# Performance work log

Hardware: AMD Instinct MI355X
Metric: run time of the kernel (lower is better)

The kernel has to match this reference:

```python
import math
import jax, jax.numpy as jnp
import numpy as np

DIM_IN = 2048
DIM_OUT = 2048
BLOCK = 128
N_BLOCKS = 256
SPARSITY = 0.1
BATCH = 8192


def setup_inputs() -> dict:
    key = jax.random.key(0)
    k1, k2, k3, k4, k5 = jax.random.split(key, 5)
    x = jax.random.normal(k1, (BATCH, DIM_IN), dtype=jnp.float32)
    weight = jax.random.normal(k2, (DIM_IN, DIM_OUT), dtype=jnp.float32) * (1.0 / math.sqrt(DIM_IN))
    bias = jax.random.normal(k3, (DIM_OUT,), dtype=jnp.float32) * 0.01
    gate_w = jax.random.normal(k4, (DIM_IN, N_BLOCKS), dtype=jnp.float32) * (1.0 / math.sqrt(DIM_IN))
    gate_b = jax.random.normal(k5, (N_BLOCKS,), dtype=jnp.float32) * 0.01
    return {"x": x, "weight": weight, "bias": bias, "gate_w": gate_w, "gate_b": gate_b}


def _sparsify1d(g):
    # k-th largest kept per row; threshold, mask, renormalize (Sparsify1D)
    n = g.shape[-1]
    k = int(math.ceil(SPARSITY * n))
    topval = jax.lax.top_k(g, k)[0][:, -1:]          # (B, 1) k-th largest value
    res = jnp.where(g >= topval, g, jnp.zeros_like(g))
    return res / (jnp.sum(res, axis=-1, keepdims=True) / n)


def reference(x, weight, bias, gate_w, gate_b):
    B = x.shape[0]
    s = DIM_IN // BLOCK                               # 16 block-rows/cols
    # gate network: Linear -> Sparsify1D
    g = _sparsify1d(x @ gate_w + gate_b)              # (B, s*s)
    gb = g.reshape(B, s, s)                           # (B, s_in, s_out)
    xb = x.reshape(B, s, BLOCK)                       # (B, s_in, block)
    Wb = weight.reshape(s, BLOCK, s, BLOCK)           # (s_in, block, s_out, block)
    # gated block matrix-vector multiply:
    # y[b,q,n] = sum_{p,m} g[b,p,q] * x[b,p,m] * W[p,m,q,n]
    y = jnp.einsum('bpq,bpm,pmqn->bqn', gb, xb, Wb)
    return y.reshape(B, DIM_OUT) + bias
```

## Files before the change

### kernel.cpp

```cpp
#include <hip/hip_runtime.h>
#include <hip/hip_bf16.h>
#include <stdint.h>

#define BATCH  8192
#define DIN    2048
#define DOUT   2048
#define NB     256
#define KSEL   26
#define GDELTA 1e-4f

typedef __attribute__((ext_vector_type(4))) float f32x4;
typedef __attribute__((ext_vector_type(8))) __bf16 bf16x8;
typedef __attribute__((ext_vector_type(8))) unsigned short u16x8;

__device__ __forceinline__ float bf2f(unsigned short u){
  union { unsigned int i; float f; } v; v.i = ((unsigned int)u) << 16; return v.f;
}
__device__ __forceinline__ unsigned short f2bf_c(float f){
  __bf16 b = (__bf16)f;
  union { __bf16 b; unsigned short u; } v; v.b = b; return v.u;
}
__device__ __forceinline__ void gload16(const unsigned short* g, unsigned short* l){
  __builtin_amdgcn_global_load_lds(
      (const __attribute__((address_space(1))) void*)g,
      (__attribute__((address_space(3))) void*)l, 16, 0, 0);
}


__global__ __launch_bounds__(256) void conv_wt2(const float* __restrict__ w,
                                                unsigned short* __restrict__ wtt)
{
  __shared__ float tl[64][65];
  const int k0 = blockIdx.x * 64;
  const int n0 = blockIdx.y * 64;
  const int c  = threadIdx.x & 63;
  const int r4 = threadIdx.x >> 6;
  #pragma unroll
  for (int i = 0; i < 16; i++){
    const int r = r4 * 16 + i;
    tl[r][c] = w[(size_t)(k0 + r) * DOUT + n0 + c];
  }
  __syncthreads();
  const int n  = threadIdx.x & 63;
  const int cp = threadIdx.x >> 6;
  const int gn = n0 + n;
  const size_t base = ((size_t)(gn >> 7) * 32 + (k0 >> 6)) * 8192 + (size_t)(gn & 127) * 64;
  const int sw = gn & 7;
  #pragma unroll
  for (int u = 0; u < 2; u++){
    const int cc = cp * 2 + u;
    u16x8 o;
    #pragma unroll
    for (int j = 0; j < 8; j++) o[j] = f2bf_c(tl[cc * 8 + j][n]);
    *(u16x8*)&wtt[base + ((cc ^ sw) << 3)] = o;
  }
}

__global__ __launch_bounds__(256) void conv_gwt2(const float* __restrict__ gw,
    unsigned short* __restrict__ ght, unsigned short* __restrict__ glt)
{
  __shared__ float tl[64][65];
  const int k0 = blockIdx.x * 64;
  const int c0 = blockIdx.y * 64;
  const int c  = threadIdx.x & 63;
  const int r4 = threadIdx.x >> 6;
  #pragma unroll
  for (int i = 0; i < 16; i++){
    const int r = r4 * 16 + i;
    tl[r][c] = gw[(size_t)(k0 + r) * NB + c0 + c];
  }
  __syncthreads();
  const int n  = threadIdx.x & 63;
  const int cp = threadIdx.x >> 6;
  const size_t base = ((size_t)(c0 >> 6) * 32 + (k0 >> 6)) * 4096 + (size_t)n * 64;
  const int sw = n & 7;
  #pragma unroll
  for (int u = 0; u < 2; u++){
    const int cc = cp * 2 + u;
    u16x8 hi, lo;
    #pragma unroll
    for (int j = 0; j < 8; j++){
      const float v = tl[cc * 8 + j][n];
      const __bf16 hb = (__bf16)v;
      union { __bf16 b; unsigned short u; } uh; uh.b = hb;
      hi[j] = uh.u;
      lo[j] = f2bf_c(v - (float)hb);
    }
    const int off = (cc ^ sw) << 3;
    *(u16x8*)&ght[base + off] = hi;
    *(u16x8*)&glt[base + off] = lo;
  }
}

__global__ __launch_bounds__(256) void gate_v3(
    const float* __restrict__ x,
    const unsigned short* __restrict__ ght,
    const unsigned short* __restrict__ glt,
    float* __restrict__ part,
    unsigned short* __restrict__ xbt)
{
  __shared__ unsigned short Axh[128 * 64], Axl[128 * 64];
  __shared__ unsigned short Bh[2][64 * 64], Bl[2][64 * 64];

  const int b0   = blockIdx.x * 128;
  const int ct   = blockIdx.y;
  const int z    = blockIdx.z;
  const int ks0  = z * 16;
  const int t    = threadIdx.x;
  const int lane = t & 63;
  const int wid  = t >> 6;
  const int bw   = wid & 1;
  const int cw   = wid >> 1;
  const int l15  = lane & 15;
  const int l4   = lane >> 4;
  const bool emit = (blockIdx.y == 0);

  const int ar  = t >> 1;
  const int ah4 = (t & 1) * 4;

  f32x4 acc[4][2];
  #pragma unroll
  for (int m = 0; m < 4; m++)
    #pragma unroll
    for (int n = 0; n < 2; n++) acc[m][n] = (f32x4)0.0f;

  int aoff[2][4], boff[2][2];
  #pragma unroll
  for (int ksi = 0; ksi < 2; ksi++){
    const int chunk = ksi * 4 + l4;
    #pragma unroll
    for (int m = 0; m < 4; m++){
      const int row = bw * 64 + m * 16 + l15;
      aoff[ksi][m] = row * 64 + ((chunk ^ (row & 7)) << 3);
    }
    #pragma unroll
    for (int n = 0; n < 2; n++){
      const int row = cw * 32 + n * 16 + l15;
      boff[ksi][n] = row * 64 + ((chunk ^ (row & 7)) << 3);
    }
  }

  f32x4 xr[8];
  auto LOADX = [&](int s){
    const float* xp = &x[(size_t)(b0 + ar) * DIN + (size_t)(ks0 + s) * 64 + ah4 * 8];
    #pragma unroll
    for (int j = 0; j < 8; j++) xr[j] = ((const f32x4*)xp)[j];
  };
  auto GLOADB = [&](int bb, int s){
    const size_t base = ((size_t)ct * 32 + (ks0 + s)) * 4096;
    #pragma unroll
    for (int i = 0; i < 2; i++){
      const int slot = (wid * 2 + i) * 512;
      gload16(ght + base + slot + lane * 8, &Bh[bb][slot]);
      gload16(glt + base + slot + lane * 8, &Bl[bb][slot]);
    }
  };
  auto WRITEA = [&](int s){
    const int sw = ar & 7;
    const size_t gb = ((size_t)(b0 >> 7) * 32 + (ks0 + s)) * 8192 + (size_t)ar * 64;
    #pragma unroll
    for (int j = 0; j < 4; j++){
      u16x8 hi, lo;
      #pragma unroll
      for (int e = 0; e < 8; e++){
        const float v = xr[j * 2 + (e >> 2)][e & 3];
        const __bf16 hb = (__bf16)v;
        union { __bf16 b; unsigned short u; } uh; uh.b = hb;
        hi[e] = uh.u;
        lo[e] = f2bf_c(v - (float)hb);
      }
      const int c8 = ((ah4 + j) ^ sw) << 3;
      *(u16x8*)&Axh[ar * 64 + c8] = hi;
      *(u16x8*)&Axl[ar * 64 + c8] = lo;
      if (emit) *(u16x8*)&xbt[gb + c8] = hi;
    }
  };

  GLOADB(0, 0);
  LOADX(0);
  int buf = 0;
  #pragma unroll 1
  for (int s = 0; s < 16; s++){
    __syncthreads();
    WRITEA(s);
    __syncthreads();
    if (s < 15){ GLOADB(buf ^ 1, s + 1); LOADX(s + 1); }
    #pragma unroll
    for (int ksi = 0; ksi < 2; ksi++){
      bf16x8 ah[4], al[4], bh[2], bl[2];
      #pragma unroll
      for (int m = 0; m < 4; m++){
        ah[m] = *(const bf16x8*)&Axh[aoff[ksi][m]];
        al[m] = *(const bf16x8*)&Axl[aoff[ksi][m]];
      }
      #pragma unroll
      for (int n = 0; n < 2; n++){
        bh[n] = *(const bf16x8*)&Bh[buf][boff[ksi][n]];
        bl[n] = *(const bf16x8*)&Bl[buf][boff[ksi][n]];
      }
      #pragma unroll
      for (int m = 0; m < 4; m++)
        #pragma unroll
        for (int n = 0; n < 2; n++){
          acc[m][n] = __builtin_amdgcn_mfma_f32_16x16x32_bf16(ah[m], bh[n], acc[m][n], 0, 0, 0);
          acc[m][n] = __builtin_amdgcn_mfma_f32_16x16x32_bf16(al[m], bh[n], acc[m][n], 0, 0, 0);
          acc[m][n] = __builtin_amdgcn_mfma_f32_16x16x32_bf16(ah[m], bl[n], acc[m][n], 0, 0, 0);
        }
    }
    buf ^= 1;
  }

  float* dst = part + (size_t)z * BATCH * NB;
  #pragma unroll
  for (int m = 0; m < 4; m++){
    const int brow = b0 + bw * 64 + m * 16 + l4 * 4;
    #pragma unroll
    for (int n = 0; n < 2; n++){
      const int ccol = ct * 64 + cw * 32 + n * 16 + l15;
      #pragma unroll
      for (int r = 0; r < 4; r++)
        dst[(size_t)(brow + r) * NB + ccol] = acc[m][n][r];
    }
  }
}

__global__ __launch_bounds__(256) void topk(float* __restrict__ part,
    const float* __restrict__ gb, int* __restrict__ flags)
{
  const int lane = threadIdx.x & 63;
  const int row  = blockIdx.x * 4 + (threadIdx.x >> 6);
  f32x4* p0 = (f32x4*)&part[(size_t)row * NB];
  const f32x4* p1 = (const f32x4*)&part[(size_t)(BATCH + row) * NB];
  const f32x4* gbv = (const f32x4*)gb;
  f32x4 v = p0[lane] + p1[lane] + gbv[lane];

  const float NEG = -3.402823466e38f;
  float w0 = v[0], w1 = v[1], w2 = v[2], w3 = v[3];
  float thr = 0.f, nxt = 0.f;
  for (int it = 0; it < KSEL + 1; it++){
    float lm = fmaxf(fmaxf(w0, w1), fmaxf(w2, w3));
    float wm = lm;
    #pragma unroll
    for (int off = 32; off; off >>= 1) wm = fmaxf(wm, __shfl_xor(wm, off, 64));
    unsigned long long ball = __ballot(lm == wm);
    int first = __ffsll(ball) - 1;
    if (lane == first){
      if      (w0 == wm) w0 = NEG;
      else if (w1 == wm) w1 = NEG;
      else if (w2 == wm) w2 = NEG;
      else               w3 = NEG;
    }
    if (it < KSEL) thr = wm; else nxt = wm;
  }
  if (lane == 0) flags[row] = (thr - nxt < GDELTA) ? 1 : 0;

  float s = 0.f;
  #pragma unroll
  for (int j = 0; j < 4; j++) s += (v[j] >= thr) ? v[j] : 0.f;
  #pragma unroll
  for (int off = 32; off; off >>= 1) s += __shfl_xor(s, off, 64);
  const float d = s * (1.0f / NB);
  f32x4 o;
  #pragma unroll
  for (int j = 0; j < 4; j++) o[j] = (v[j] >= thr) ? v[j] / d : 0.f;
  p0[lane] = o;
}

__global__ __launch_bounds__(256) void refine(
    const float* __restrict__ x, const float* __restrict__ gw,
    const float* __restrict__ gb, const int* __restrict__ flags,
    float* __restrict__ part)
{
  const int lane = threadIdx.x & 63;
  const int row  = blockIdx.x * 4 + (threadIdx.x >> 6);
  if (!flags[row]) return;

  f32x4 acc0 = (f32x4)0.f, acc1 = (f32x4)0.f;
  const float* xp = &x[(size_t)row * DIN];
  #pragma unroll 8
  for (int k = 0; k < 1024; k++){
    const float xv = xp[k];
    const f32x4 wv = *(const f32x4*)&gw[(size_t)k * NB + lane * 4];
    #pragma unroll
    for (int j = 0; j < 4; j++) acc0[j] = fmaf(xv, wv[j], acc0[j]);
  }
  #pragma unroll 8
  for (int k = 1024; k < 2048; k++){
    const float xv = xp[k];
    const f32x4 wv = *(const f32x4*)&gw[(size_t)k * NB + lane * 4];
    #pragma unroll
    for (int j = 0; j < 4; j++) acc1[j] = fmaf(xv, wv[j], acc1[j]);
  }
  const f32x4 gbv = *(const f32x4*)&gb[lane * 4];
  f32x4 v;
  #pragma unroll
  for (int j = 0; j < 4; j++) v[j] = acc0[j] + acc1[j] + gbv[j];

  const float NEG = -3.402823466e38f;
  float w0 = v[0], w1 = v[1], w2 = v[2], w3 = v[3];
  float thr = 0.f;
  for (int it = 0; it < KSEL; it++){
    float lm = fmaxf(fmaxf(w0, w1), fmaxf(w2, w3));
    float wm = lm;
    #pragma unroll
    for (int off = 32; off; off >>= 1) wm = fmaxf(wm, __shfl_xor(wm, off, 64));
    unsigned long long ball = __ballot(lm == wm);
    int first = __ffsll(ball) - 1;
    if (lane == first){
      if      (w0 == wm) w0 = NEG;
      else if (w1 == wm) w1 = NEG;
      else if (w2 == wm) w2 = NEG;
      else               w3 = NEG;
    }
    thr = wm;
  }
  float s = 0.f;
  #pragma unroll
  for (int j = 0; j < 4; j++) s += (v[j] >= thr) ? v[j] : 0.f;
  #pragma unroll
  for (int off = 32; off; off >>= 1) s += __shfl_xor(s, off, 64);
  const float d = s * (1.0f / NB);
  f32x4 o;
  #pragma unroll
  for (int j = 0; j < 4; j++) o[j] = (v[j] >= thr) ? v[j] / d : 0.f;
  *(f32x4*)&part[(size_t)row * NB + lane * 4] = o;
}

__global__ __launch_bounds__(256) void main_v3(
    const unsigned short* __restrict__ xbt,
    const unsigned short* __restrict__ wtt,
    const float* __restrict__ g,
    const float* __restrict__ bias,
    float* __restrict__ out)
{
  __shared__ unsigned short XA[2][128 * 64], WB[2][128 * 64];
  __shared__ float gl[128 * 17];

  const int f  = blockIdx.x;
  const int q  = f >> 6;
  const int bt = (f & 7) * 8 + ((f >> 3) & 7);
  const int b0 = bt * 128;
  const int t    = threadIdx.x;
  const int lane = t & 63;
  const int wid  = t >> 6;
  const int wr   = (wid >> 1) * 64;
  const int wc   = (wid & 1) * 64;
  const int l15  = lane & 15;
  const int l4   = lane >> 4;

  for (int e = t; e < 128 * 16; e += 256){
    const int r = e >> 4, p = e & 15;
    gl[r * 17 + p] = g[(size_t)(b0 + r) * NB + p * 16 + q];
  }

  f32x4 accT[4][4], accP[4][4];
  #pragma unroll
  for (int m = 0; m < 4; m++)
    #pragma unroll
    for (int n = 0; n < 4; n++){ accT[m][n] = (f32x4)0.0f; accP[m][n] = (f32x4)0.0f; }

  int aoff[2][4], boff[2][4];
  #pragma unroll
  for (int ksi = 0; ksi < 2; ksi++){
    const int chunk = ksi * 4 + l4;
    #pragma unroll
    for (int m = 0; m < 4; m++){
      const int row = wr + m * 16 + l15;
      aoff[ksi][m] = row * 64 + ((chunk ^ (row & 7)) << 3);
    }
    #pragma unroll
    for (int n = 0; n < 4; n++){
      const int row = wc + n * 16 + l15;
      boff[ksi][n] = row * 64 + ((chunk ^ (row & 7)) << 3);
    }
  }

  const unsigned short* asrc0 = xbt + (size_t)bt * 32 * 8192;
  const unsigned short* bsrc0 = wtt + (size_t)q  * 32 * 8192;

  auto GLOAD = [&](int bb, int kp){
    const unsigned short* as = asrc0 + (size_t)kp * 8192;
    const unsigned short* bs = bsrc0 + (size_t)kp * 8192;
    #pragma unroll
    for (int i = 0; i < 4; i++){
      const int slot = (wid * 4 + i) * 512;
      gload16(as + slot + lane * 8, &XA[bb][slot]);
      gload16(bs + slot + lane * 8, &WB[bb][slot]);
    }
  };

  GLOAD(0, 0);
  int buf = 0;
  #pragma unroll 1
  for (int kp = 0; kp < 32; kp++){
    __syncthreads();
    if (kp < 31) GLOAD(buf ^ 1, kp + 1);
    #pragma unroll
    for (int ksi = 0; ksi < 2; ksi++){
      bf16x8 a[4], b[4];
      #pragma unroll
      for (int m = 0; m < 4; m++) a[m] = *(const bf16x8*)&XA[buf][aoff[ksi][m]];
      #pragma unroll
      for (int n = 0; n < 4; n++) b[n] = *(const bf16x8*)&WB[buf][boff[ksi][n]];
      #pragma unroll
      for (int m = 0; m < 4; m++)
        #pragma unroll
        for (int n = 0; n < 4; n++)
          accP[m][n] = __builtin_amdgcn_mfma_f32_16x16x32_bf16(a[m], b[n], accP[m][n], 0, 0, 0);
    }
    if (kp & 1){
      const int p = kp >> 1;
      #pragma unroll
      for (int m = 0; m < 4; m++){
        const int rb = wr + m * 16 + l4 * 4;
        f32x4 g4;
        #pragma unroll
        for (int r = 0; r < 4; r++) g4[r] = gl[(rb + r) * 17 + p];
        #pragma unroll
        for (int n = 0; n < 4; n++){
          accT[m][n] += g4 * accP[m][n];
          accP[m][n] = (f32x4)0.0f;
        }
      }
    }
    buf ^= 1;
  }

  #pragma unroll
  for (int n = 0; n < 4; n++){
    const int col = q * 128 + wc + n * 16 + l15;
    const float bv = bias[col];
    #pragma unroll
    for (int m = 0; m < 4; m++){
      #pragma unroll
      for (int r = 0; r < 4; r++){
        const int row = b0 + wr + m * 16 + l4 * 4 + r;
        out[(size_t)row * DOUT + col] = accT[m][n][r] + bv;
      }
    }
  }
}

extern "C" void kernel_launch(void* const* d_in, const int* in_sizes, int n_in,
                              void* d_out, int out_size, void* d_ws, size_t ws_size,
                              hipStream_t stream)
{
  const float* x    = (const float*)d_in[0];
  const float* w    = (const float*)d_in[1];
  const float* bias = (const float*)d_in[2];
  const float* gw   = (const float*)d_in[3];
  const float* gb   = (const float*)d_in[4];
  float* out = (float*)d_out;

  char* wsb = (char*)d_ws;
  float*          part = (float*)wsb;
  unsigned short* wtt  = (unsigned short*)(wsb + (size_t)8  * 1024 * 1024);
  unsigned short* xbt  = (unsigned short*)(wsb + (size_t)16 * 1024 * 1024);
  unsigned short* ght  = (unsigned short*)(wsb + (size_t)48 * 1024 * 1024);
  unsigned short* glt  = (unsigned short*)(wsb + (size_t)49 * 1024 * 1024);
  int*            flg  = (int*)           (wsb + (size_t)50 * 1024 * 1024);

  conv_gwt2<<<dim3(DIN / 64, NB / 64), 256, 0, stream>>>(gw, ght, glt);
  gate_v3  <<<dim3(BATCH / 128, 4, 2), 256, 0, stream>>>(x, ght, glt, part, xbt);
  topk     <<<BATCH / 4, 256, 0, stream>>>(part, gb, flg);
  refine   <<<BATCH / 4, 256, 0, stream>>>(x, gw, gb, flg, part);
  conv_wt2 <<<dim3(DIN / 64, DOUT / 64), 256, 0, stream>>>(w, wtt);
  main_v3  <<<1024, 256, 0, stream>>>(xbt, wtt, part, bias, out);
}
```

Baseline: 288.3 us.

## Pre-split x into bf16 hi/lo tiles and switch to 32-wide K tiles

Adds a separate conversion kernel that splits x into bf16 hi and lo tiles in a swizzled 32-wide K layout, storing the lo part temporarily in the output buffer. The gate GEMM then streams both operands with direct global-to-LDS loads instead of converting in registers, which removes one barrier per step. All tiled layouts (weight, gate weight, x) move to 32-element K chunks with a new swizzle. The main kernel applies the gate per 128-wide block through a transposed gate tile in LDS, read as one vector load. In exchange it adds a kernel launch, an extra global round trip for the x lo part, and twice as many K iterations with smaller tiles.

```diff
diff --git a/kernel.cpp b/kernel.cpp
--- a/kernel.cpp
+++ b/kernel.cpp
@@ -27,6 +27,37 @@
 }
 
 
+__global__ __launch_bounds__(256) void conv_xhl(const float* __restrict__ x,
+    unsigned short* __restrict__ xht, unsigned short* __restrict__ xlt)
+{
+  const int r    = threadIdx.x >> 2;
+  const int cq   = threadIdx.x & 3;
+  const int grow = blockIdx.x * 64 + r;
+  const int kp   = (blockIdx.y << 2) + cq;
+  const int lrow = grow & 127;
+  const int sw   = (lrow >> 1) & 3;
+  const size_t base = ((size_t)(grow >> 7) * 64 + kp) * 4096 + lrow * 32;
+  const float* xp = &x[(size_t)grow * DIN + kp * 32];
+  #pragma unroll
+  for (int c3 = 0; c3 < 4; c3++){
+    f32x4 a0 = *(const f32x4*)(xp + c3 * 8);
+    f32x4 a1 = *(const f32x4*)(xp + c3 * 8 + 4);
+    u16x8 hi, lo;
+    #pragma unroll
+    for (int j = 0; j < 4; j++){
+      const __bf16 h0 = (__bf16)a0[j];
+      const __bf16 h1 = (__bf16)a1[j];
+      union { __bf16 b; unsigned short u; } u0, u1; u0.b = h0; u1.b = h1;
+      hi[j] = u0.u; hi[4 + j] = u1.u;
+      lo[j]     = f2bf_c(a0[j] - (float)h0);
+      lo[4 + j] = f2bf_c(a1[j] - (float)h1);
+    }
+    const int off = (c3 ^ sw) << 3;
+    *(u16x8*)&xht[base + off] = hi;
+    *(u16x8*)&xlt[base + off] = lo;
+  }
+}
+
 __global__ __launch_bounds__(256) void conv_wt2(const float* __restrict__ w,
                                                 unsigned short* __restrict__ wtt)
 {
@@ -44,15 +75,18 @@
   const int n  = threadIdx.x & 63;
   const int cp = threadIdx.x >> 6;
   const int gn = n0 + n;
-  const size_t base = ((size_t)(gn >> 7) * 32 + (k0 >> 6)) * 8192 + (size_t)(gn & 127) * 64;
-  const int sw = gn & 7;
+  const int q  = gn >> 7;
+  const int ln = gn & 127;
+  const int sw = (ln >> 1) & 3;
   #pragma unroll
   for (int u = 0; u < 2; u++){
     const int cc = cp * 2 + u;
+    const int kp = (k0 >> 5) + (cc >> 2);
+    const int c3 = cc & 3;
     u16x8 o;
     #pragma unroll
     for (int j = 0; j < 8; j++) o[j] = f2bf_c(tl[cc * 8 + j][n]);
-    *(u16x8*)&wtt[base + ((cc ^ sw) << 3)] = o;
+    *(u16x8*)&wtt[((size_t)q * 64 + kp) * 4096 + ln * 32 + ((c3 ^ sw) << 3)] = o;
   }
 }
 
@@ -70,42 +104,45 @@
     tl[r][c] = gw[(size_t)(k0 + r) * NB + c0 + c];
   }
   __syncthreads();
-  const int n  = threadIdx.x & 63;
+  const int ln = threadIdx.x & 63;
   const int cp = threadIdx.x >> 6;
-  const size_t base = ((size_t)(c0 >> 6) * 32 + (k0 >> 6)) * 4096 + (size_t)n * 64;
-  const int sw = n & 7;
+  const int ct = blockIdx.y;
+  const int sw = (ln >> 1) & 3;
   #pragma unroll
   for (int u = 0; u < 2; u++){
     const int cc = cp * 2 + u;
+    const int kp = (k0 >> 5) + (cc >> 2);
+    const int c3 = cc & 3;
     u16x8 hi, lo;
     #pragma unroll
     for (int j = 0; j < 8; j++){
-      const float v = tl[cc * 8 + j][n];
+      const float v = tl[cc * 8 + j][ln];
       const __bf16 hb = (__bf16)v;
       union { __bf16 b; unsigned short u; } uh; uh.b = hb;
       hi[j] = uh.u;
       lo[j] = f2bf_c(v - (float)hb);
     }
-    const int off = (cc ^ sw) << 3;
+    const size_t base = ((size_t)ct * 64 + kp) * 2048 + ln * 32;
+    const int off = (c3 ^ sw) << 3;
     *(u16x8*)&ght[base + off] = hi;
     *(u16x8*)&glt[base + off] = lo;
   }
 }
 
-__global__ __launch_bounds__(256) void gate_v3(
-    const float* __restrict__ x,
+__global__ __launch_bounds__(256) void gate_v5(
+    const unsigned short* __restrict__ xht,
+    const unsigned short* __restrict__ xlt,
     const unsigned short* __restrict__ ght,
     const unsigned short* __restrict__ glt,
-    float* __restrict__ part,
-    unsigned short* __restrict__ xbt)
-{
-  __shared__ unsigned short Axh[128 * 64], Axl[128 * 64];
-  __shared__ unsigned short Bh[2][64 * 64], Bl[2][64 * 64];
-
-  const int b0   = blockIdx.x * 128;
+    float* __restrict__ part)
+{
+  __shared__ unsigned short Ah[2][4096], Al[2][4096];
+  __shared__ unsigned short Bh[2][2048], Bl[2][2048];
+
+  const int bt   = blockIdx.x;
+  const int b0   = bt * 128;
   const int ct   = blockIdx.y;
   const int z    = blockIdx.z;
-  const int ks0  = z * 16;
   const int t    = threadIdx.x;
   const int lane = t & 63;
   const int wid  = t >> 6;
@@ -113,10 +150,11 @@
   const int cw   = wid >> 1;
   const int l15  = lane & 15;
   const int l4   = lane >> 4;
-  const bool emit = (blockIdx.y == 0);
-
-  const int ar  = t >> 1;
-  const int ah4 = (t & 1) * 4;
+
+  const unsigned short* axh = xht + ((size_t)bt * 64 + z * 32) * 4096;
+  const unsigned short* axl = xlt + ((size_t)bt * 64 + z * 32) * 4096;
+  const unsigned short* bgh = ght + ((size_t)ct * 64 + z * 32) * 2048;
+  const unsigned short* bgl = glt + ((size_t)ct * 64 + z * 32) * 2048;
 
   f32x4 acc[4][2];
   #pragma unroll
@@ -124,89 +162,55 @@
     #pragma unroll
     for (int n = 0; n < 2; n++) acc[m][n] = (f32x4)0.0f;
 
-  int aoff[2][4], boff[2][2];
-  #pragma unroll
-  for (int ksi = 0; ksi < 2; ksi++){
-    const int chunk = ksi * 4 + l4;
-    #pragma unroll
-    for (int m = 0; m < 4; m++){
-      const int row = bw * 64 + m * 16 + l15;
-      aoff[ksi][m] = row * 64 + ((chunk ^ (row & 7)) << 3);
-    }
-    #pragma unroll
-    for (int n = 0; n < 2; n++){
-      const int row = cw * 32 + n * 16 + l15;
-      boff[ksi][n] = row * 64 + ((chunk ^ (row & 7)) << 3);
-    }
-  }
-
-  f32x4 xr[8];
-  auto LOADX = [&](int s){
-    const float* xp = &x[(size_t)(b0 + ar) * DIN + (size_t)(ks0 + s) * 64 + ah4 * 8];
-    #pragma unroll
-    for (int j = 0; j < 8; j++) xr[j] = ((const f32x4*)xp)[j];
+  int aoff[4], boff[2];
+  #pragma unroll
+  for (int m = 0; m < 4; m++){
+    const int row = bw * 64 + m * 16 + l15;
+    aoff[m] = row * 32 + ((l4 ^ ((row >> 1) & 3)) << 3);
+  }
+  #pragma unroll
+  for (int n = 0; n < 2; n++){
+    const int row = cw * 32 + n * 16 + l15;
+    boff[n] = row * 32 + ((l4 ^ ((row >> 1) & 3)) << 3);
+  }
+
+  auto GLOAD = [&](int bb, int s){
+    #pragma unroll
+    for (int i = 0; i < 2; i++){
+      const int sl = (wid * 2 + i) * 512;
+      gload16(axh + (size_t)s * 4096 + sl + lane * 8, &Ah[bb][sl]);
+      gload16(axl + (size_t)s * 4096 + sl + lane * 8, &Al[bb][sl]);
+    }
+    const int slb = wid * 512;
+    gload16(bgh + (size_t)s * 2048 + slb + lane * 8, &Bh[bb][slb]);
+    gload16(bgl + (size_t)s * 2048 + slb + lane * 8, &Bl[bb][slb]);
   };
-  auto GLOADB = [&](int bb, int s){
-    const size_t base = ((size_t)ct * 32 + (ks0 + s)) * 4096;
-    #pragma unroll
-    for (int i = 0; i < 2; i++){
-      const int slot = (wid * 2 + i) * 512;
-      gload16(ght + base + slot + lane * 8, &Bh[bb][slot]);
-      gload16(glt + base + slot + lane * 8, &Bl[bb][slot]);
-    }
-  };
-  auto WRITEA = [&](int s){
-    const int sw = ar & 7;
-    const size_t gb = ((size_t)(b0 >> 7) * 32 + (ks0 + s)) * 8192 + (size_t)ar * 64;
-    #pragma unroll
-    for (int j = 0; j < 4; j++){
-      u16x8 hi, lo;
-      #pragma unroll
-      for (int e = 0; e < 8; e++){
-        const float v = xr[j * 2 + (e >> 2)][e & 3];
-        const __bf16 hb = (__bf16)v;
-        union { __bf16 b; unsigned short u; } uh; uh.b = hb;
-        hi[e] = uh.u;
-        lo[e] = f2bf_c(v - (float)hb);
-      }
-      const int c8 = ((ah4 + j) ^ sw) << 3;
-      *(u16x8*)&Axh[ar * 64 + c8] = hi;
-      *(u16x8*)&Axl[ar * 64 + c8] = lo;
-      if (emit) *(u16x8*)&xbt[gb + c8] = hi;
-    }
-  };
-
-  GLOADB(0, 0);
-  LOADX(0);
+
+  GLOAD(0, 0);
   int buf = 0;
   #pragma unroll 1
-  for (int s = 0; s < 16; s++){
+  for (int s = 0; s < 32; s++){
     __syncthreads();
-    WRITEA(s);
-    __syncthreads();
-    if (s < 15){ GLOADB(buf ^ 1, s + 1); LOADX(s + 1); }
-    #pragma unroll
-    for (int ksi = 0; ksi < 2; ksi++){
-      bf16x8 ah[4], al[4], bh[2], bl[2];
-      #pragma unroll
-      for (int m = 0; m < 4; m++){
-        ah[m] = *(const bf16x8*)&Axh[aoff[ksi][m]];
-        al[m] = *(const bf16x8*)&Axl[aoff[ksi][m]];
+    if (s < 31) GLOAD(buf ^ 1, s + 1);
+    bf16x8 ah[4], al[4], bh[2], bl[2];
+    #pragma unroll
+    for (int m = 0; m < 4; m++){
+      ah[m] = *(const bf16x8*)&Ah[buf][aoff[m]];
+      al[m] = *(const bf16x8*)&Al[buf][aoff[m]];
+    }
+    #pragma unroll
+    for (int n = 0; n < 2; n++){
+      bh[n] = *(const bf16x8*)&Bh[buf][boff[n]];
+      bl[n] = *(const bf16x8*)&Bl[buf][boff[n]];
+    }
+    #pragma unroll
+    for (int m = 0; m < 4; m++)
+      #pragma unroll
+      for (int n = 0; n < 2; n++){
+        acc[m][n] = __builtin_amdgcn_mfma_f32_16x16x32_bf16(ah[m], bh[n], acc[m][n], 0, 0, 0);
+        acc[m][n] = __builtin_amdgcn_mfma_f32_16x16x32_bf16(al[m], bh[n], acc[m][n], 0, 0, 0);
+        acc[m][n] = __builtin_amdgcn_mfma_f32_16x16x32_bf16(ah[m], bl[n], acc[m][n], 0, 0, 0);
       }
-      #pragma unroll
-      for (int n = 0; n < 2; n++){
-        bh[n] = *(const bf16x8*)&Bh[buf][boff[ksi][n]];
-        bl[n] = *(const bf16x8*)&Bl[buf][boff[ksi][n]];
-      }
-      #pragma unroll
-      for (int m = 0; m < 4; m++)
-        #pragma unroll
-        for (int n = 0; n < 2; n++){
-          acc[m][n] = __builtin_amdgcn_mfma_f32_16x16x32_bf16(ah[m], bh[n], acc[m][n], 0, 0, 0);
-          acc[m][n] = __builtin_amdgcn_mfma_f32_16x16x32_bf16(al[m], bh[n], acc[m][n], 0, 0, 0);
-          acc[m][n] = __builtin_amdgcn_mfma_f32_16x16x32_bf16(ah[m], bl[n], acc[m][n], 0, 0, 0);
-        }
-    }
     buf ^= 1;
   }
 
@@ -326,15 +330,15 @@
   *(f32x4*)&part[(size_t)row * NB + lane * 4] = o;
 }
 
-__global__ __launch_bounds__(256) void main_v3(
-    const unsigned short* __restrict__ xbt,
+__global__ __launch_bounds__(256) void main_v4(
+    const unsigned short* __restrict__ xht,
     const unsigned short* __restrict__ wtt,
     const float* __restrict__ g,
     const float* __restrict__ bias,
     float* __restrict__ out)
 {
-  __shared__ unsigned short XA[2][128 * 64], WB[2][128 * 64];
-  __shared__ float gl[128 * 17];
+  __shared__ unsigned short XA[2][4096], WB[2][4096];
+  __shared__ float gl2[16 * 132];
 
   const int f  = blockIdx.x;
   const int q  = f >> 6;
@@ -348,82 +352,81 @@
   const int l15  = lane & 15;
   const int l4   = lane >> 4;
 
-  for (int e = t; e < 128 * 16; e += 256){
-    const int r = e >> 4, p = e & 15;
-    gl[r * 17 + p] = g[(size_t)(b0 + r) * NB + p * 16 + q];
-  }
-
-  f32x4 accT[4][4], accP[4][4];
+  for (int e = t; e < 16 * 128; e += 256){
+    const int p = e >> 7, r = e & 127;
+    gl2[p * 132 + r] = g[(size_t)(b0 + r) * NB + p * 16 + q];
+  }
+
+  f32x4 accT[4][4];
   #pragma unroll
   for (int m = 0; m < 4; m++)
     #pragma unroll
-    for (int n = 0; n < 4; n++){ accT[m][n] = (f32x4)0.0f; accP[m][n] = (f32x4)0.0f; }
-
-  int aoff[2][4], boff[2][4];
-  #pragma unroll
-  for (int ksi = 0; ksi < 2; ksi++){
-    const int chunk = ksi * 4 + l4;
-    #pragma unroll
-    for (int m = 0; m < 4; m++){
-      const int row = wr + m * 16 + l15;
-      aoff[ksi][m] = row * 64 + ((chunk ^ (row & 7)) << 3);
-    }
-    #pragma unroll
-    for (int n = 0; n < 4; n++){
-      const int row = wc + n * 16 + l15;
-      boff[ksi][n] = row * 64 + ((chunk ^ (row & 7)) << 3);
-    }
-  }
-
-  const unsigned short* asrc0 = xbt + (size_t)bt * 32 * 8192;
-  const unsigned short* bsrc0 = wtt + (size_t)q  * 32 * 8192;
+    for (int n = 0; n < 4; n++) accT[m][n] = (f32x4)0.0f;
+  const f32x4 z4 = (f32x4)0.0f;
+
+  int aoff[4], boff[4];
+  #pragma unroll
+  for (int m = 0; m < 4; m++){
+    const int row = wr + m * 16 + l15;
+    aoff[m] = row * 32 + ((l4 ^ ((row >> 1) & 3)) << 3);
+  }
+  #pragma unroll
+  for (int n = 0; n < 4; n++){
+    const int row = wc + n * 16 + l15;
+    boff[n] = row * 32 + ((l4 ^ ((row >> 1) & 3)) << 3);
+  }
+
+  const unsigned short* asrc0 = xht + (size_t)bt * 64 * 4096;
+  const unsigned short* bsrc0 = wtt + (size_t)q  * 64 * 4096;
 
   auto GLOAD = [&](int bb, int kp){
-    const unsigned short* as = asrc0 + (size_t)kp * 8192;
-    const unsigned short* bs = bsrc0 + (size_t)kp * 8192;
-    #pragma unroll
-    for (int i = 0; i < 4; i++){
-      const int slot = (wid * 4 + i) * 512;
-      gload16(as + slot + lane * 8, &XA[bb][slot]);
-      gload16(bs + slot + lane * 8, &WB[bb][slot]);
+    const unsigned short* as = asrc0 + (size_t)kp * 4096;
+    const unsigned short* bs = bsrc0 + (size_t)kp * 4096;
+    #pragma unroll
+    for (int i = 0; i < 2; i++){
+      const int sl = (wid * 2 + i) * 512;
+      gload16(as + sl + lane * 8, &XA[bb][sl]);
+      gload16(bs + sl + lane * 8, &WB[bb][sl]);
     }
   };
 
   GLOAD(0, 0);
   int buf = 0;
   #pragma unroll 1
-  for (int kp = 0; kp < 32; kp++){
-    __syncthreads();
-    if (kp < 31) GLOAD(buf ^ 1, kp + 1);
-    #pragma unroll
-    for (int ksi = 0; ksi < 2; ksi++){
+  for (int pb = 0; pb < 16; pb++){
+    f32x4 accP[4][4];
+    #pragma unroll
+    for (int s4 = 0; s4 < 4; s4++){
+      const int kp = pb * 4 + s4;
+      __syncthreads();
+      if (kp < 63) GLOAD(buf ^ 1, kp + 1);
       bf16x8 a[4], b[4];
       #pragma unroll
-      for (int m = 0; m < 4; m++) a[m] = *(const bf16x8*)&XA[buf][aoff[ksi][m]];
-      #pragma unroll
-      for (int n = 0; n < 4; n++) b[n] = *(const bf16x8*)&WB[buf][boff[ksi][n]];
-      #pragma unroll
-      for (int m = 0; m < 4; m++)
+      for (int m = 0; m < 4; m++) a[m] = *(const bf16x8*)&XA[buf][aoff[m]];
+      #pragma unroll
+      for (int n = 0; n < 4; n++) b[n] = *(const bf16x8*)&WB[buf][boff[n]];
+      if (s4 == 0){
         #pragma unroll
-        for (int n = 0; n < 4; n++)
-          accP[m][n] = __builtin_amdgcn_mfma_f32_16x16x32_bf16(a[m], b[n], accP[m][n], 0, 0, 0);
-    }
-    if (kp & 1){
-      const int p = kp >> 1;
-      #pragma unroll
-      for (int m = 0; m < 4; m++){
-        const int rb = wr + m * 16 + l4 * 4;
-        f32x4 g4;
+        for (int m = 0; m < 4; m++)
+          #pragma unroll
+          for (int n = 0; n < 4; n++)
+            accP[m][n] = __builtin_amdgcn_mfma_f32_16x16x32_bf16(a[m], b[n], z4, 0, 0, 0);
+      } else {
         #pragma unroll
-        for (int r = 0; r < 4; r++) g4[r] = gl[(rb + r) * 17 + p];
-        #pragma unroll
-        for (int n = 0; n < 4; n++){
-          accT[m][n] += g4 * accP[m][n];
-          accP[m][n] = (f32x4)0.0f;
-        }
+        for (int m = 0; m < 4; m++)
+          #pragma unroll
+          for (int n = 0; n < 4; n++)
+            accP[m][n] = __builtin_amdgcn_mfma_f32_16x16x32_bf16(a[m], b[n], accP[m][n], 0, 0, 0);
       }
-    }
-    buf ^= 1;
+      buf ^= 1;
+    }
+    #pragma unroll
+    for (int m = 0; m < 4; m++){
+      const f32x4 g4 = *(const f32x4*)&gl2[pb * 132 + wr + m * 16 + l4 * 4];
+      #pragma unroll
+      for (int n = 0; n < 4; n++)
+        accT[m][n] += g4 * accP[m][n];
+    }
   }
 
   #pragma unroll
@@ -455,15 +458,17 @@
   char* wsb = (char*)d_ws;
   float*          part = (float*)wsb;
   unsigned short* wtt  = (unsigned short*)(wsb + (size_t)8  * 1024 * 1024);
-  unsigned short* xbt  = (unsigned short*)(wsb + (size_t)16 * 1024 * 1024);
+  unsigned short* xht  = (unsigned short*)(wsb + (size_t)16 * 1024 * 1024);
   unsigned short* ght  = (unsigned short*)(wsb + (size_t)48 * 1024 * 1024);
   unsigned short* glt  = (unsigned short*)(wsb + (size_t)49 * 1024 * 1024);
   int*            flg  = (int*)           (wsb + (size_t)50 * 1024 * 1024);
-
+  unsigned short* xlt  = (unsigned short*)d_out;
+
+  conv_xhl <<<dim3(BATCH / 64, DIN / 128), 256, 0, stream>>>(x, xht, xlt);
   conv_gwt2<<<dim3(DIN / 64, NB / 64), 256, 0, stream>>>(gw, ght, glt);
-  gate_v3  <<<dim3(BATCH / 128, 4, 2), 256, 0, stream>>>(x, ght, glt, part, xbt);
+  gate_v5  <<<dim3(BATCH / 128, NB / 64, 2), 256, 0, stream>>>(xht, xlt, ght, glt, part);
   topk     <<<BATCH / 4, 256, 0, stream>>>(part, gb, flg);
   refine   <<<BATCH / 4, 256, 0, stream>>>(x, gw, gb, flg, part);
   conv_wt2 <<<dim3(DIN / 64, DOUT / 64), 256, 0, stream>>>(w, wtt);
-  main_v3  <<<1024, 256, 0, stream>>>(xbt, wtt, part, bias, out);
-}
+  main_v4  <<<1024, 256, 0, stream>>>(xht, wtt, part, bias, out);
+}
```

Result: slower. 305.9 us (+6.1%).
